# Performance work log

Measured on AMD Instinct MI355X. Metric: run time of the kernel, lower is better.

The kernel has to match this reference:

```python
import jax, jax.numpy as jnp
import numpy as np

B, S, DM, H, HD = 2, 4096, 768, 12, 64
SCALING = HD ** -0.5
LN_EPS = 1e-12
ROPE_BASE = 10000.0


def rotate_half(x):
    x1, x2 = jnp.split(x, 2, axis=-1)
    return jnp.concatenate([-x2, x1], axis=-1)


def setup_inputs() -> dict:
    key = jax.random.key(0)
    ks = jax.random.split(key, 8)
    s = 0.02
    hidden_states = jax.random.normal(ks[0], (B, S, DM), dtype=jnp.float32)
    # true rotary tables: inv_freq over head_dim/2, duplicated (HF convention)
    inv_freq = 1.0 / (ROPE_BASE ** (jnp.arange(0, HD, 2, dtype=jnp.float32) / HD))
    freqs = jnp.arange(S, dtype=jnp.float32)[:, None] * inv_freq[None, :]  # [S, HD/2]
    emb = jnp.concatenate([freqs, freqs], axis=-1)                          # [S, HD]
    cos, sin = jnp.cos(emb), jnp.sin(emb)
    return {
        "hidden_states": hidden_states,
        "cos": cos,
        "sin": sin,
        "Wq": jax.random.normal(ks[1], (DM, DM), dtype=jnp.float32) * s,
        "bq": jnp.zeros((DM,), dtype=jnp.float32),
        "Wk": jax.random.normal(ks[2], (DM, DM), dtype=jnp.float32) * s,
        "bk": jnp.zeros((DM,), dtype=jnp.float32),
        "Wv": jax.random.normal(ks[3], (DM, DM), dtype=jnp.float32) * s,
        "bv": jnp.zeros((DM,), dtype=jnp.float32),
        "Wo": jax.random.normal(ks[4], (DM, DM), dtype=jnp.float32) * s,
        "ln_g": jnp.ones((DM,), dtype=jnp.float32),
        "ln_b": jnp.zeros((DM,), dtype=jnp.float32),
    }


def reference(hidden_states, cos, sin, Wq, bq, Wk, bk, Wv, bv, Wo, ln_g, ln_b):
    # QKV projections -> [B, H, S, HD]
    def proj(W, b):
        return (hidden_states @ W.T + b).reshape(B, S, H, HD).transpose(0, 2, 1, 3)
    q, k, v = proj(Wq, bq), proj(Wk, bk), proj(Wv, bv)

    # RoPE (cos/sin broadcast over batch & heads)
    c = cos[None, None, :, :]
    s_ = sin[None, None, :, :]
    q = q * c + rotate_half(q) * s_
    k = k * c + rotate_half(k) * s_

    # Faithful to source: q pre-scaled, then eager attention scales scores again
    q = q * SCALING
    scores = jnp.einsum("bhsd,bhtd->bhst", q, k) * SCALING  # [B,H,S,S]
    probs = jax.nn.softmax(scores.astype(jnp.float32), axis=-1).astype(v.dtype)
    attn = jnp.einsum("bhst,bhtd->bhsd", probs, v)
    attn = attn.transpose(0, 2, 1, 3).reshape(B, S, DM)

    # output dense (no bias) + residual + LayerNorm
    out = attn @ Wo.T + hidden_states
    mu = jnp.mean(out, axis=-1, keepdims=True)
    var = jnp.var(out, axis=-1, keepdims=True)
    out = (out - mu) * jax.lax.rsqrt(var + LN_EPS) * ln_g + ln_b
    return out
```

## Files before the change

kernel.cpp:

```cpp
#include <hip/hip_runtime.h>
#include <math.h>

#define B_   2
#define S_   4096
#define DM_  768
#define H_   12
#define HD_  64
#define M_   (B_ * S_)
#define ROWELEMS ((size_t)M_ * DM_)
#define WELEMS  ((size_t)DM_ * DM_)

#define QSC (1.4426950408889634f / 64.0f)

typedef unsigned short u16;
typedef unsigned int   u32;
typedef __attribute__((ext_vector_type(8))) short  short8;
typedef __attribute__((ext_vector_type(4))) float  floatx4;

__device__ inline u16 f2bf(float f) {
    u32 u = __builtin_bit_cast(u32, f);
    u += 0x7FFF + ((u >> 16) & 1);
    return (u16)(u >> 16);
}
__device__ inline float bf2f(u16 h) {
    return __builtin_bit_cast(float, (u32)h << 16);
}
__device__ inline u32 pk_trunc(float a, float b) {
    return __builtin_amdgcn_perm(__builtin_bit_cast(u32, b),
                                 __builtin_bit_cast(u32, a), 0x07060302);
}

__device__ inline int sw_off(int r, int cg) {
    return (r << 6) + ((cg ^ (r & 7)) << 3);
}

__device__ __forceinline__ void load_lds16(const u16* g, u16* l) {
    __builtin_amdgcn_global_load_lds(
        (const __attribute__((address_space(1))) u32*)g,
        (__attribute__((address_space(3))) u32*)l, 16, 0, 0);
}

__device__ __forceinline__ void drain_vm() {
    __builtin_amdgcn_s_waitcnt(0x0F70);
}

__global__ __launch_bounds__(256) void conv_bf16(
    const float* __restrict__ h,  const float* __restrict__ wq,
    const float* __restrict__ wk, const float* __restrict__ wv,
    const float* __restrict__ wo, u16* __restrict__ hb, u16* __restrict__ wb)
{
    const int y = blockIdx.y;
    const float* src; u16* dst; size_t n4;
    if (y == 0)      { src = h;  dst = hb;              n4 = ROWELEMS / 4; }
    else if (y == 1) { src = wq; dst = wb;              n4 = WELEMS / 4; }
    else if (y == 2) { src = wk; dst = wb + WELEMS;     n4 = WELEMS / 4; }
    else if (y == 3) { src = wv; dst = wb + 2 * WELEMS; n4 = WELEMS / 4; }
    else             { src = wo; dst = wb + 3 * WELEMS; n4 = WELEMS / 4; }
    const size_t stride = (size_t)gridDim.x * 256;
    for (size_t i = blockIdx.x * 256 + threadIdx.x; i < n4; i += stride) {
        float4 v = *(const float4*)&src[i * 4];
        u32 p0 = (u32)f2bf(v.x) | ((u32)f2bf(v.y) << 16);
        u32 p1 = (u32)f2bf(v.z) | ((u32)f2bf(v.w) << 16);
        *(uint2*)&dst[i * 4] = make_uint2(p0, p1);
    }
}

__global__ __launch_bounds__(256, 3) void gemm_qkv(
    const u16* __restrict__ A,
    const u16* __restrict__ W0, const u16* __restrict__ W1, const u16* __restrict__ W2,
    const float* __restrict__ b0, const float* __restrict__ b1, const float* __restrict__ b2,
    const float* __restrict__ cosT, const float* __restrict__ sinT,
    u16* __restrict__ Qh, u16* __restrict__ Kh, u16* __restrict__ Vt)
{
    __shared__ __align__(16) u16 As[128 * 64];
    __shared__ __align__(16) u16 Ws[128 * 64];

    const int tid  = threadIdx.x;
    const int wave = tid >> 6, lane = tid & 63;
    const int n16  = lane & 15, quad = lane >> 4;
    const int wm   = wave >> 1, wn = wave & 1;
    const int m0   = blockIdx.y * 128, n0 = blockIdx.x * 128;
    const int z    = blockIdx.z;

    const u16* Wz = (z == 0) ? W0 : (z == 1) ? W1 : W2;
    const float* bz = (z == 0) ? b0 : (z == 1) ? b1 : b2;

    int gao[4], ldso[4];
#pragma unroll
    for (int i = 0; i < 4; i++) {
        int g = wave * 256 + i * 64 + lane;
        int r = g >> 3, cg = (g & 7) ^ (r & 7);
        gao[i]  = r * DM_ + cg * 8;
        ldso[i] = (wave * 256 + i * 64) * 8;
    }
    const u16* Ap = A  + (size_t)m0 * DM_;
    const u16* Wp = Wz + (size_t)n0 * DM_;

    floatx4 acc[4][4];
#pragma unroll
    for (int i = 0; i < 4; i++)
#pragma unroll
        for (int j = 0; j < 4; j++) acc[i][j] = (floatx4){0.f, 0.f, 0.f, 0.f};

    for (int k0 = 0; k0 < DM_; k0 += 64) {
        __syncthreads();
#pragma unroll
        for (int i = 0; i < 4; i++) {
            load_lds16(Ap + k0 + gao[i], &As[ldso[i]]);
            load_lds16(Wp + k0 + gao[i], &Ws[ldso[i]]);
        }
        drain_vm();
        __syncthreads();
#pragma unroll
        for (int ks = 0; ks < 2; ks++) {
            short8 af[4], bf[4];
#pragma unroll
            for (int t = 0; t < 4; t++) {
                af[t] = *(const short8*)&As[sw_off(wm * 64 + t * 16 + n16, ks * 4 + quad)];
                bf[t] = *(const short8*)&Ws[sw_off(wn * 64 + t * 16 + n16, ks * 4 + quad)];
            }
#pragma unroll
            for (int i = 0; i < 4; i++)
#pragma unroll
                for (int j = 0; j < 4; j++)
                    acc[i][j] = __builtin_amdgcn_mfma_f32_16x16x32_bf16(
                        af[i], bf[j], acc[i][j], 0, 0, 0);
        }
    }

    if (z == 2) {
#pragma unroll
        for (int i = 0; i < 4; i++)
#pragma unroll
            for (int j = 0; j < 4; j++) {
                const int col = n0 + wn * 64 + j * 16 + n16;
                const int h = col >> 6, hd = col & 63;
                const int row0 = m0 + wm * 64 + i * 16 + quad * 4;
                const int b = row0 >> 12, s0 = row0 & 4095;
                const float bias = bz[col];
                float v0 = acc[i][j][0] + bias, v1 = acc[i][j][1] + bias;
                float v2 = acc[i][j][2] + bias, v3 = acc[i][j][3] + bias;
                u32 w0 = (u32)f2bf(v0) | ((u32)f2bf(v1) << 16);
                u32 w1 = (u32)f2bf(v2) | ((u32)f2bf(v3) << 16);
                *(uint2*)&Vt[((size_t)(b * H_ + h) * HD_ + hd) * S_ + s0] = make_uint2(w0, w1);
            }
    } else {
        u32* Out32 = (u32*)((z == 0) ? Qh : Kh);
        const float sc_ = (z == 0) ? QSC : 1.0f;
#pragma unroll
        for (int i = 0; i < 4; i++)
#pragma unroll
            for (int j = 0; j < 2; j++) {
                const int col1 = n0 + wn * 64 + j * 16 + n16;
                const int col2 = col1 + 32;
                const int h = col1 >> 6, hd1 = col1 & 63;
                const float bias1 = bz[col1], bias2 = bz[col2];
#pragma unroll
                for (int r = 0; r < 4; r++) {
                    const int row = m0 + wm * 64 + i * 16 + quad * 4 + r;
                    const int b = row >> 12, s = row & 4095;
                    const float c  = cosT[s * HD_ + hd1];
                    const float sn = sinT[s * HD_ + hd1];
                    const float x1 = acc[i][j][r] + bias1;
                    const float x2 = acc[i][j + 2][r] + bias2;
                    const float y1 = (x1 * c - x2 * sn) * sc_;
                    const float y2 = (x2 * c + x1 * sn) * sc_;
                    Out32[(((size_t)(b * H_ + h) * S_ + s) << 5) + hd1] =
                        (u32)f2bf(y1) | ((u32)f2bf(y2) << 16);
                }
            }
    }
}

__global__ __launch_bounds__(256, 4) void flash_mfma(
    const u16* __restrict__ Qh, const u16* __restrict__ Kh,
    const u16* __restrict__ Vt, u16* __restrict__ O)
{
    __shared__ __align__(16) u16 Ks[64 * 64];
    __shared__ __align__(16) u16 Vs[64 * 64];
    __shared__ __align__(16) u16 Ps[128 * 64];

    const int tid  = threadIdx.x;
    const int wave = tid >> 6, lane = tid & 63;
    const int n16  = lane & 15, quad = lane >> 4;
    const int qt   = blockIdx.x;
    const int bh   = blockIdx.y;
    const size_t qk_base = (size_t)bh * S_ * HD_;
    const size_t vt_base = (size_t)bh * HD_ * S_;
    const int q0   = qt * 128;
    const int wrow = wave * 32;

    short8 qf[2][2];
#pragma unroll
    for (int rt = 0; rt < 2; rt++)
#pragma unroll
        for (int ks = 0; ks < 2; ks++)
            qf[rt][ks] = *(const short8*)&Qh[qk_base +
                (size_t)(q0 + wrow + rt * 16 + n16) * HD_ + ks * 32 + quad * 8];

    short8 ones;
#pragma unroll
    for (int j = 0; j < 8; j++) ones[j] = (short)0x3F80;

    int gk_off[2], gv_off[2], ldso[2];
#pragma unroll
    for (int i = 0; i < 2; i++) {
        int g = wave * 128 + i * 64 + lane;
        int r = g >> 3, cg = (g & 7) ^ (r & 7);
        gk_off[i] = r * HD_ + cg * 8;
        gv_off[i] = r * S_  + cg * 8;
        ldso[i]   = (wave * 128 + i * 64) * 8;
    }

    floatx4 o_acc[2][4];
    floatx4 o_l[2];
#pragma unroll
    for (int rt = 0; rt < 2; rt++) {
        o_l[rt] = (floatx4){0.f, 0.f, 0.f, 0.f};
#pragma unroll
        for (int dt = 0; dt < 4; dt++) o_acc[rt][dt] = (floatx4){0.f, 0.f, 0.f, 0.f};
    }

    const u16* Kg = Kh + qk_base;
    const u16* Vg = Vt + vt_base;

    for (int kt = 0; kt < 64; kt++) {
        __syncthreads();
#pragma unroll
        for (int i = 0; i < 2; i++) {
            load_lds16(Kg + gk_off[i], &Ks[ldso[i]]);
            load_lds16(Vg + gv_off[i], &Vs[ldso[i]]);
        }
        drain_vm();
        __syncthreads();
        Kg += 64 * HD_;
        Vg += 64;

        floatx4 sct[4][2];
#pragma unroll
        for (int ct = 0; ct < 4; ct++)
#pragma unroll
            for (int rt = 0; rt < 2; rt++)
                sct[ct][rt] = (floatx4){0.f, 0.f, 0.f, 0.f};
#pragma unroll
        for (int ks = 0; ks < 2; ks++) {
            short8 kf[4];
#pragma unroll
            for (int ct = 0; ct < 4; ct++)
                kf[ct] = *(const short8*)&Ks[sw_off(ct * 16 + n16, ks * 4 + quad)];
#pragma unroll
            for (int ct = 0; ct < 4; ct++)
#pragma unroll
                for (int rt = 0; rt < 2; rt++)
                    sct[ct][rt] = __builtin_amdgcn_mfma_f32_16x16x32_bf16(
                        kf[ct], qf[rt][ks], sct[ct][rt], 0, 0, 0);
        }

#pragma unroll
        for (int rt = 0; rt < 2; rt++)
#pragma unroll
            for (int ct = 0; ct < 4; ct++) {
                float p0 = __builtin_amdgcn_exp2f(sct[ct][rt][0]);
                float p1 = __builtin_amdgcn_exp2f(sct[ct][rt][1]);
                float p2 = __builtin_amdgcn_exp2f(sct[ct][rt][2]);
                float p3 = __builtin_amdgcn_exp2f(sct[ct][rt][3]);
                uint2 w = make_uint2(pk_trunc(p0, p1), pk_trunc(p2, p3));
                const int row = wrow + rt * 16 + n16;
                const int off = sw_off(row, ct * 2 + (quad >> 1)) + (quad & 1) * 4;
                *(uint2*)&Ps[off] = w;
            }

#pragma unroll
        for (int ks = 0; ks < 2; ks++) {
            short8 pa[2];
#pragma unroll
            for (int rt = 0; rt < 2; rt++)
                pa[rt] = *(const short8*)&Ps[sw_off(wrow + rt * 16 + n16, ks * 4 + quad)];
            short8 vb[4];
#pragma unroll
            for (int dt = 0; dt < 4; dt++)
                vb[dt] = *(const short8*)&Vs[sw_off(dt * 16 + n16, ks * 4 + quad)];
#pragma unroll
            for (int rt = 0; rt < 2; rt++) {
#pragma unroll
                for (int dt = 0; dt < 4; dt++)
                    o_acc[rt][dt] = __builtin_amdgcn_mfma_f32_16x16x32_bf16(
                        pa[rt], vb[dt], o_acc[rt][dt], 0, 0, 0);
                o_l[rt] = __builtin_amdgcn_mfma_f32_16x16x32_bf16(
                    pa[rt], ones, o_l[rt], 0, 0, 0);
            }
        }
    }

    const int b = bh / H_, h = bh % H_;
#pragma unroll
    for (int rt = 0; rt < 2; rt++)
#pragma unroll
        for (int r = 0; r < 4; r++) {
            const float inv = 1.0f / o_l[rt][r];
            const int srow = q0 + wrow + rt * 16 + quad * 4 + r;
            u16* Orow = O + ((size_t)b * S_ + srow) * DM_ + h * HD_;
#pragma unroll
            for (int dt = 0; dt < 4; dt++)
                Orow[dt * 16 + n16] = f2bf(o_acc[rt][dt][r] * inv);
        }
}

__global__ __launch_bounds__(256, 4) void gemm_out(
    const u16* __restrict__ A, const u16* __restrict__ W,
    const float* __restrict__ resid, float* __restrict__ Cf)
{
    __shared__ __align__(16) u16 As[64 * 64];
    __shared__ __align__(16) u16 Ws[128 * 64];

    const int tid  = threadIdx.x;
    const int wave = tid >> 6, lane = tid & 63;
    const int n16  = lane & 15, quad = lane >> 4;
    const int wm   = wave >> 1, wn = wave & 1;
    const int m0   = blockIdx.y * 64, n0 = blockIdx.x * 128;

    int gwo[4], ldswo[4], gao[2], ldsao[2];
#pragma unroll
    for (int i = 0; i < 4; i++) {
        int g = wave * 256 + i * 64 + lane;
        int r = g >> 3, cg = (g & 7) ^ (r & 7);
        gwo[i]   = r * DM_ + cg * 8;
        ldswo[i] = (wave * 256 + i * 64) * 8;
    }
#pragma unroll
    for (int i = 0; i < 2; i++) {
        int g = wave * 128 + i * 64 + lane;
        int r = g >> 3, cg = (g & 7) ^ (r & 7);
        gao[i]   = r * DM_ + cg * 8;
        ldsao[i] = (wave * 128 + i * 64) * 8;
    }
    const u16* Wp = W + (size_t)n0 * DM_;
    const u16* Ap = A + (size_t)m0 * DM_;

    floatx4 acc[2][4];
#pragma unroll
    for (int i = 0; i < 2; i++)
#pragma unroll
        for (int j = 0; j < 4; j++) acc[i][j] = (floatx4){0.f, 0.f, 0.f, 0.f};

    for (int k0 = 0; k0 < DM_; k0 += 64) {
        __syncthreads();
#pragma unroll
        for (int i = 0; i < 4; i++)
            load_lds16(Wp + k0 + gwo[i], &Ws[ldswo[i]]);
#pragma unroll
        for (int i = 0; i < 2; i++)
            load_lds16(Ap + k0 + gao[i], &As[ldsao[i]]);
        drain_vm();
        __syncthreads();

#pragma unroll
        for (int ks = 0; ks < 2; ks++) {
            short8 af[2], bf[4];
#pragma unroll
            for (int rt = 0; rt < 2; rt++)
                af[rt] = *(const short8*)&As[sw_off(wm * 32 + rt * 16 + n16, ks * 4 + quad)];
#pragma unroll
            for (int ct = 0; ct < 4; ct++)
                bf[ct] = *(const short8*)&Ws[sw_off(wn * 64 + ct * 16 + n16, ks * 4 + quad)];
#pragma unroll
            for (int rt = 0; rt < 2; rt++)
#pragma unroll
                for (int ct = 0; ct < 4; ct++)
                    acc[rt][ct] = __builtin_amdgcn_mfma_f32_16x16x32_bf16(
                        af[rt], bf[ct], acc[rt][ct], 0, 0, 0);
        }
    }

#pragma unroll
    for (int rt = 0; rt < 2; rt++)
#pragma unroll
        for (int ct = 0; ct < 4; ct++) {
            const int col = n0 + wn * 64 + ct * 16 + n16;
#pragma unroll
            for (int r = 0; r < 4; r++) {
                const int row = m0 + wm * 32 + rt * 16 + quad * 4 + r;
                Cf[(size_t)row * DM_ + col] = acc[rt][ct][r] + resid[(size_t)row * DM_ + col];
            }
        }
}

__global__ __launch_bounds__(256) void ln_kernel(
    float* __restrict__ io, const float* __restrict__ g, const float* __restrict__ bb)
{
    const int row = blockIdx.x, t = threadIdx.x;
    float* p = io + (size_t)row * DM_;
    float x[3];
    float sum = 0.0f, sq = 0.0f;
#pragma unroll
    for (int i = 0; i < 3; i++) {
        x[i] = p[t + i * 256];
        sum += x[i];
        sq  = fmaf(x[i], x[i], sq);
    }
#pragma unroll
    for (int off = 32; off >= 1; off >>= 1) {
        sum += __shfl_xor(sum, off);
        sq  += __shfl_xor(sq, off);
    }
    __shared__ float s1[4], s2[4];
    if ((t & 63) == 0) { s1[t >> 6] = sum; s2[t >> 6] = sq; }
    __syncthreads();
    sum = s1[0] + s1[1] + s1[2] + s1[3];
    sq  = s2[0] + s2[1] + s2[2] + s2[3];
    const float mu  = sum * (1.0f / 768.0f);
    const float var = sq * (1.0f / 768.0f) - mu * mu;
    const float rs  = rsqrtf(var + 1e-12f);
#pragma unroll
    for (int i = 0; i < 3; i++) {
        const int c = t + i * 256;
        p[c] = (x[i] - mu) * rs * g[c] + bb[c];
    }
}

extern "C" void kernel_launch(void* const* d_in, const int* in_sizes, int n_in,
                              void* d_out, int out_size, void* d_ws, size_t ws_size,
                              hipStream_t stream)
{
    const float* hidden = (const float*)d_in[0];
    const float* cosT   = (const float*)d_in[1];
    const float* sinT   = (const float*)d_in[2];
    const float* Wq     = (const float*)d_in[3];
    const float* bq     = (const float*)d_in[4];
    const float* Wk     = (const float*)d_in[5];
    const float* bk     = (const float*)d_in[6];
    const float* Wv     = (const float*)d_in[7];
    const float* bv     = (const float*)d_in[8];
    const float* Wo     = (const float*)d_in[9];
    const float* ln_g   = (const float*)d_in[10];
    const float* ln_b   = (const float*)d_in[11];
    float* out = (float*)d_out;

    u16* wsb = (u16*)d_ws;
    u16* Hb  = wsb;
    u16* Wb  = wsb + ROWELEMS;
    u16* Qh  = Wb + 4 * WELEMS;
    u16* Kh  = Qh + ROWELEMS;
    u16* Vt  = Kh + ROWELEMS;
    u16* Ob  = Hb;
    u16* Wqb = Wb, *Wkb = Wb + WELEMS, *Wvb = Wb + 2 * WELEMS, *Wob = Wb + 3 * WELEMS;

    conv_bf16<<<dim3(1024, 5), 256, 0, stream>>>(hidden, Wq, Wk, Wv, Wo, Hb, Wb);

    gemm_qkv<<<dim3(DM_ / 128, M_ / 128, 3), 256, 0, stream>>>(
        Hb, Wqb, Wkb, Wvb, bq, bk, bv, cosT, sinT, Qh, Kh, Vt);

    flash_mfma<<<dim3(S_ / 128, B_ * H_), 256, 0, stream>>>(Qh, Kh, Vt, Ob);

    gemm_out<<<dim3(DM_ / 128, M_ / 64), 256, 0, stream>>>(Ob, Wob, hidden, out);

    ln_kernel<<<M_, 256, 0, stream>>>(out, ln_g, ln_b);
}
```

Baseline: 295.7 us.

## Double-buffer K/V tiles in flash attention to overlap loads with MFMA

Splits the K and V shared-memory tiles into two buffers. The next tile's global-to-LDS loads are issued before computing on the current one, and a partial vmcnt wait is used instead of a full drain. This hides global load latency behind the QK and PV MFMA work. It costs 16KB more LDS, which may lower occupancy under the 4-block launch bound. It also switches to raw s_barrier, which needs correct LDS ordering with the Ps writes.

```diff
diff --git a/kernel.cpp b/kernel.cpp
--- a/kernel.cpp
+++ b/kernel.cpp
@@ -42,6 +42,9 @@
 
 __device__ __forceinline__ void drain_vm() {
     __builtin_amdgcn_s_waitcnt(0x0F70);
+}
+__device__ __forceinline__ void wait_vm4() {
+    __builtin_amdgcn_s_waitcnt(0x0F74);
 }
 
 __global__ __launch_bounds__(256) void conv_bf16(
@@ -176,8 +179,8 @@
     const u16* __restrict__ Qh, const u16* __restrict__ Kh,
     const u16* __restrict__ Vt, u16* __restrict__ O)
 {
-    __shared__ __align__(16) u16 Ks[64 * 64];
-    __shared__ __align__(16) u16 Vs[64 * 64];
+    __shared__ __align__(16) u16 Ks[2][64 * 64];
+    __shared__ __align__(16) u16 Vs[2][64 * 64];
     __shared__ __align__(16) u16 Ps[128 * 64];
 
     const int tid  = threadIdx.x;
@@ -224,17 +227,27 @@
     const u16* Kg = Kh + qk_base;
     const u16* Vg = Vt + vt_base;
 
+#pragma unroll
+    for (int i = 0; i < 2; i++) {
+        load_lds16(Kg + gk_off[i], &Ks[0][ldso[i]]);
+        load_lds16(Vg + gv_off[i], &Vs[0][ldso[i]]);
+    }
+
     for (int kt = 0; kt < 64; kt++) {
-        __syncthreads();
-#pragma unroll
-        for (int i = 0; i < 2; i++) {
-            load_lds16(Kg + gk_off[i], &Ks[ldso[i]]);
-            load_lds16(Vg + gv_off[i], &Vs[ldso[i]]);
-        }
-        drain_vm();
-        __syncthreads();
-        Kg += 64 * HD_;
-        Vg += 64;
+        const int cur = kt & 1;
+        if (kt + 1 < 64) {
+            const u16* Kg1 = Kg + (size_t)(kt + 1) * (64 * HD_);
+            const u16* Vg1 = Vg + (kt + 1) * 64;
+#pragma unroll
+            for (int i = 0; i < 2; i++) {
+                load_lds16(Kg1 + gk_off[i], &Ks[cur ^ 1][ldso[i]]);
+                load_lds16(Vg1 + gv_off[i], &Vs[cur ^ 1][ldso[i]]);
+            }
+            wait_vm4();
+        } else {
+            drain_vm();
+        }
+        __builtin_amdgcn_s_barrier();
 
         floatx4 sct[4][2];
 #pragma unroll
@@ -247,7 +260,7 @@
             short8 kf[4];
 #pragma unroll
             for (int ct = 0; ct < 4; ct++)
-                kf[ct] = *(const short8*)&Ks[sw_off(ct * 16 + n16, ks * 4 + quad)];
+                kf[ct] = *(const short8*)&Ks[cur][sw_off(ct * 16 + n16, ks * 4 + quad)];
 #pragma unroll
             for (int ct = 0; ct < 4; ct++)
 #pragma unroll
@@ -279,7 +292,7 @@
             short8 vb[4];
 #pragma unroll
             for (int dt = 0; dt < 4; dt++)
-                vb[dt] = *(const short8*)&Vs[sw_off(dt * 16 + n16, ks * 4 + quad)];
+                vb[dt] = *(const short8*)&Vs[cur][sw_off(dt * 16 + n16, ks * 4 + quad)];
 #pragma unroll
             for (int rt = 0; rt < 2; rt++) {
 #pragma unroll
@@ -290,6 +303,8 @@
                     pa[rt], ones, o_l[rt], 0, 0, 0);
             }
         }
+
+        __builtin_amdgcn_s_barrier();
     }
 
     const int b = bh / H_, h = bh % H_;
```

Result: slower. 307.4 us (+4.0%).

## Load K and V fragments directly from global memory instead of LDS staging

Applied to the files above, without the earlier changes.

The flash attention kernel no longer stages K and V tiles through shared memory with cooperative async loads and two syncthreads per iteration. Each wave now reads its MFMA operand fragments straight from global memory, relying on cache hits across waves, and uses a single raw barrier per tile. The occupancy hint drops from 4 to 3 blocks to allow more registers. This removes LDS traffic and sync stalls, but every wave issues redundant global loads and exposes their latency without prefetching. The Ps write/read hazard is still guarded only by s_barrier at the loop top, which relies on the compiler's waitcnt handling.

```diff
diff --git a/kernel.cpp b/kernel.cpp
--- a/kernel.cpp
+++ b/kernel.cpp
@@ -172,12 +172,10 @@
     }
 }
 
-__global__ __launch_bounds__(256, 4) void flash_mfma(
+__global__ __launch_bounds__(256, 3) void flash_mfma(
     const u16* __restrict__ Qh, const u16* __restrict__ Kh,
     const u16* __restrict__ Vt, u16* __restrict__ O)
 {
-    __shared__ __align__(16) u16 Ks[64 * 64];
-    __shared__ __align__(16) u16 Vs[64 * 64];
     __shared__ __align__(16) u16 Ps[128 * 64];
 
     const int tid  = threadIdx.x;
@@ -202,16 +200,6 @@
 #pragma unroll
     for (int j = 0; j < 8; j++) ones[j] = (short)0x3F80;
 
-    int gk_off[2], gv_off[2], ldso[2];
-#pragma unroll
-    for (int i = 0; i < 2; i++) {
-        int g = wave * 128 + i * 64 + lane;
-        int r = g >> 3, cg = (g & 7) ^ (r & 7);
-        gk_off[i] = r * HD_ + cg * 8;
-        gv_off[i] = r * S_  + cg * 8;
-        ldso[i]   = (wave * 128 + i * 64) * 8;
-    }
-
     floatx4 o_acc[2][4];
     floatx4 o_l[2];
 #pragma unroll
@@ -221,20 +209,11 @@
         for (int dt = 0; dt < 4; dt++) o_acc[rt][dt] = (floatx4){0.f, 0.f, 0.f, 0.f};
     }
 
-    const u16* Kg = Kh + qk_base;
-    const u16* Vg = Vt + vt_base;
+    const u16* Kp = Kh + qk_base + (size_t)n16 * HD_ + quad * 8;
+    const u16* Vp = Vt + vt_base + (size_t)n16 * S_  + quad * 8;
 
     for (int kt = 0; kt < 64; kt++) {
-        __syncthreads();
-#pragma unroll
-        for (int i = 0; i < 2; i++) {
-            load_lds16(Kg + gk_off[i], &Ks[ldso[i]]);
-            load_lds16(Vg + gv_off[i], &Vs[ldso[i]]);
-        }
-        drain_vm();
-        __syncthreads();
-        Kg += 64 * HD_;
-        Vg += 64;
+        __builtin_amdgcn_s_barrier();
 
         floatx4 sct[4][2];
 #pragma unroll
@@ -247,7 +226,7 @@
             short8 kf[4];
 #pragma unroll
             for (int ct = 0; ct < 4; ct++)
-                kf[ct] = *(const short8*)&Ks[sw_off(ct * 16 + n16, ks * 4 + quad)];
+                kf[ct] = *(const short8*)&Kp[(ct * 16) * HD_ + ks * 32];
 #pragma unroll
             for (int ct = 0; ct < 4; ct++)
 #pragma unroll
@@ -279,7 +258,7 @@
             short8 vb[4];
 #pragma unroll
             for (int dt = 0; dt < 4; dt++)
-                vb[dt] = *(const short8*)&Vs[sw_off(dt * 16 + n16, ks * 4 + quad)];
+                vb[dt] = *(const short8*)&Vp[(dt * 16) * S_ + ks * 32];
 #pragma unroll
             for (int rt = 0; rt < 2; rt++) {
 #pragma unroll
@@ -290,6 +269,9 @@
                     pa[rt], ones, o_l[rt], 0, 0, 0);
             }
         }
+
+        Kp += 64 * HD_;
+        Vp += 64;
     }
 
     const int b = bh / H_, h = bh % H_;
```

Result: slower. 524.1 us (+77.2%).

## Keep softmax probabilities in registers by permuting K rows to match MFMA layout

Applied to the files above, without the earlier changes.

The K tile rows are permuted as they are loaded into shared memory. This makes the S=K·Q^T accumulator layout line up with the A-operand layout of the P·V MFMA, so exp2'd probabilities can be packed directly into register fragments. That removes the Ps shared-memory round trip (stores, loads and LDS footprint). The occupancy hint is lowered from 4 to 3 blocks, trading occupancy for register headroom.

```diff
diff --git a/kernel.cpp b/kernel.cpp
--- a/kernel.cpp
+++ b/kernel.cpp
@@ -16,6 +16,7 @@
 typedef unsigned int   u32;
 typedef __attribute__((ext_vector_type(8))) short  short8;
 typedef __attribute__((ext_vector_type(4))) float  floatx4;
+typedef __attribute__((ext_vector_type(4))) u32    uint32x4;
 
 __device__ inline u16 f2bf(float f) {
     u32 u = __builtin_bit_cast(u32, f);
@@ -172,13 +173,12 @@
     }
 }
 
-__global__ __launch_bounds__(256, 4) void flash_mfma(
+__global__ __launch_bounds__(256, 3) void flash_mfma(
     const u16* __restrict__ Qh, const u16* __restrict__ Kh,
     const u16* __restrict__ Vt, u16* __restrict__ O)
 {
     __shared__ __align__(16) u16 Ks[64 * 64];
     __shared__ __align__(16) u16 Vs[64 * 64];
-    __shared__ __align__(16) u16 Ps[128 * 64];
 
     const int tid  = threadIdx.x;
     const int wave = tid >> 6, lane = tid & 63;
@@ -207,8 +207,9 @@
     for (int i = 0; i < 2; i++) {
         int g = wave * 128 + i * 64 + lane;
         int r = g >> 3, cg = (g & 7) ^ (r & 7);
-        gk_off[i] = r * HD_ + cg * 8;
-        gv_off[i] = r * S_  + cg * 8;
+        int rk = (r & 0x23) | ((r & 8) << 1) | ((r & 4) << 1) | ((r & 16) >> 2);
+        gk_off[i] = rk * HD_ + cg * 8;
+        gv_off[i] = r  * S_  + cg * 8;
         ldso[i]   = (wave * 128 + i * 64) * 8;
     }
 
@@ -256,26 +257,27 @@
                         kf[ct], qf[rt][ks], sct[ct][rt], 0, 0, 0);
         }
 
+        short8 pa[2][2];
 #pragma unroll
         for (int rt = 0; rt < 2; rt++)
 #pragma unroll
-            for (int ct = 0; ct < 4; ct++) {
-                float p0 = __builtin_amdgcn_exp2f(sct[ct][rt][0]);
-                float p1 = __builtin_amdgcn_exp2f(sct[ct][rt][1]);
-                float p2 = __builtin_amdgcn_exp2f(sct[ct][rt][2]);
-                float p3 = __builtin_amdgcn_exp2f(sct[ct][rt][3]);
-                uint2 w = make_uint2(pk_trunc(p0, p1), pk_trunc(p2, p3));
-                const int row = wrow + rt * 16 + n16;
-                const int off = sw_off(row, ct * 2 + (quad >> 1)) + (quad & 1) * 4;
-                *(uint2*)&Ps[off] = w;
+            for (int ks = 0; ks < 2; ks++) {
+                const floatx4 lo = sct[2 * ks][rt];
+                const floatx4 hi = sct[2 * ks + 1][rt];
+                uint32x4 w;
+                w[0] = pk_trunc(__builtin_amdgcn_exp2f(lo[0]),
+                                __builtin_amdgcn_exp2f(lo[1]));
+                w[1] = pk_trunc(__builtin_amdgcn_exp2f(lo[2]),
+                                __builtin_amdgcn_exp2f(lo[3]));
+                w[2] = pk_trunc(__builtin_amdgcn_exp2f(hi[0]),
+                                __builtin_amdgcn_exp2f(hi[1]));
+                w[3] = pk_trunc(__builtin_amdgcn_exp2f(hi[2]),
+                                __builtin_amdgcn_exp2f(hi[3]));
+                pa[rt][ks] = __builtin_bit_cast(short8, w);
             }
 
 #pragma unroll
         for (int ks = 0; ks < 2; ks++) {
-            short8 pa[2];
-#pragma unroll
-            for (int rt = 0; rt < 2; rt++)
-                pa[rt] = *(const short8*)&Ps[sw_off(wrow + rt * 16 + n16, ks * 4 + quad)];
             short8 vb[4];
 #pragma unroll
             for (int dt = 0; dt < 4; dt++)
@@ -285,9 +287,9 @@
 #pragma unroll
                 for (int dt = 0; dt < 4; dt++)
                     o_acc[rt][dt] = __builtin_amdgcn_mfma_f32_16x16x32_bf16(
-                        pa[rt], vb[dt], o_acc[rt][dt], 0, 0, 0);
+                        pa[rt][ks], vb[dt], o_acc[rt][dt], 0, 0, 0);
                 o_l[rt] = __builtin_amdgcn_mfma_f32_16x16x32_bf16(
-                    pa[rt], ones, o_l[rt], 0, 0, 0);
+                    pa[rt][ks], ones, o_l[rt], 0, 0, 0);
             }
         }
     }
```

After: 269.1 us. -9.0%, faster.
